# Optimization experiments

Hardware: AMD Instinct MI355X
Metric: run time of the kernel (lower is better)

The kernel has to match this reference:

```python
import jax, jax.numpy as jnp
import numpy as np

N_EMBD = 2048
NUM_GROUPS = 8
EXPERTS_PER_GROUP = 8
ROUTER_TEMPERATURE = 1.0
N_TOKENS = 16384


def setup_inputs() -> dict:
    key = jax.random.key(0)
    kx, kg, ke = jax.random.split(key, 3)
    x = jax.random.normal(kx, (N_TOKENS, N_EMBD), dtype=jnp.float32)
    # nn.Linear(in, out, bias=False) stores weight as [out, in]; kaiming-uniform-ish scale
    bound = 1.0 / np.sqrt(N_EMBD)
    group_gate_w = jax.random.uniform(kg, (NUM_GROUPS, N_EMBD), dtype=jnp.float32,
                                      minval=-bound, maxval=bound)
    expert_gate_w = jax.random.uniform(ke, (NUM_GROUPS * EXPERTS_PER_GROUP, N_EMBD),
                                       dtype=jnp.float32, minval=-bound, maxval=bound)
    return {"x": x, "group_gate_w": group_gate_w, "expert_gate_w": expert_gate_w}


def reference(x, group_gate_w, expert_gate_w):
    N = x.shape[0]
    G = NUM_GROUPS
    E_g = EXPERTS_PER_GROUP
    inv_temp = 1.0 / ROUTER_TEMPERATURE

    # Level 1: group routing
    group_logits = jnp.einsum('nd,gd->ng', x, group_gate_w)            # [N, G]
    group_probs = jax.nn.softmax(group_logits * inv_temp, axis=-1)     # [N, G]
    group_mask = group_probs >= (1.0 / G)                              # [N, G]

    # Level 2: expert routing within each group
    expert_logits = jnp.einsum('nd,ed->ne', x, expert_gate_w)          # [N, G*E_g]
    expert_logits = expert_logits.reshape(N, G, E_g)
    expert_probs = jax.nn.softmax(expert_logits * inv_temp, axis=-1)   # [N, G, E_g]
    expert_mask = expert_probs >= (1.0 / E_g)                          # [N, G, E_g]

    valid_mask_3d = group_mask[:, :, None] & expert_mask               # [N, G, E_g]
    selected_weights_3d = (group_probs[:, :, None] * expert_probs) * valid_mask_3d.astype(x.dtype)

    valid_mask = valid_mask_3d.reshape(N, G * E_g)
    selected_weights = selected_weights_3d.reshape(N, G * E_g)
    weight_sum = jnp.clip(jnp.sum(selected_weights, axis=-1, keepdims=True), 1e-9, None)
    normalized_weights = selected_weights / weight_sum
    return (valid_mask, normalized_weights)
```

## Files before the change

kernel.cpp:

```cpp
#include <hip/hip_runtime.h>


#define NT 16384
#define NE 2048
#define NTH 256
#define NBLK 512
#define NCHUNK 16
#define KSB 10240
#define WCH 40960
#define LDS_BYTES 81920

typedef _Float16 v8h __attribute__((ext_vector_type(8)));
typedef float    v4f __attribute__((ext_vector_type(4)));

__global__ __launch_bounds__(256, 1)
void prep(const float* __restrict__ gw, const float* __restrict__ ew,
          _Float16* __restrict__ wf)
{
    const int t = blockIdx.x * 256 + threadIdx.x;
    const int j    = t & 7;
    const int sl   = (t >> 3) & 63;
    const int rest = t >> 9;
    const int g    = rest % 5;
    const int ks   = rest / 5;
    const int m = sl & 15, q = sl >> 4;
    const int gate = g * 16 + m;
    const int k = ks * 32 + q * 8 + j;
    float v = 0.f;
    if (gate < 64)      v = ew[gate * NE + k];
    else if (gate < 72) v = gw[(gate - 64) * NE + k];
    const _Float16 h = (_Float16)v;
    const int o = (((ks * 5 + g) * 2) * 64 + sl) * 8 + j;
    wf[o]       = h;
    wf[o + 512] = (_Float16)((v - (float)h) * 2048.0f);
}

__global__ __launch_bounds__(NTH, 2)
void router(const float* __restrict__ x, const _Float16* __restrict__ wf,
            float* __restrict__ out)
{
    __shared__ __align__(16) char sm[LDS_BYTES];
    const int tid  = threadIdx.x;
    const int lane = tid & 63;
    const int w    = tid >> 6;
    const int t0   = blockIdx.x * 32;

    const float* xq0 = x + (size_t)(t0 + (lane & 15)) * NE + w * 32 + (lane >> 4) * 8;
    const float* xq1 = xq0 + (size_t)16 * NE;

    auto stage = [&](int c, int buf) {
        const char* src = (const char*)wf + (size_t)c * WCH + w * KSB + lane * 16;
        char* dst = sm + buf * WCH + w * KSB;
        #pragma unroll
        for (int i = 0; i < 10; ++i)
            __builtin_amdgcn_global_load_lds(
                (const __attribute__((address_space(1))) char*)(src + i * 1024),
                (__attribute__((address_space(3))) char*)(dst + i * 1024),
                16, 0, 0);
    };

    auto split8 = [](const float4& a, const float4& b, v8h& h, v8h& l) {
        const float v[8] = {a.x, a.y, a.z, a.w, b.x, b.y, b.z, b.w};
        #pragma unroll
        for (int j = 0; j < 8; ++j) {
            const _Float16 hh = (_Float16)v[j];
            h[j] = hh;
            l[j] = (_Float16)((v[j] - (float)hh) * 2048.0f);
        }
    };

    v4f accH0[5], accC0[5], accH1[5], accC1[5];
    #pragma unroll
    for (int g = 0; g < 5; ++g) {
        accH0[g] = (v4f)(0.f); accC0[g] = (v4f)(0.f);
        accH1[g] = (v4f)(0.f); accC1[g] = (v4f)(0.f);
    }

    auto xload = [&](int c, float4& a0, float4& a1, float4& b0, float4& b1) {
        const float* p0 = xq0 + c * 128;
        const float* p1 = xq1 + c * 128;
        a0 = *(const float4*)(p0); a1 = *(const float4*)(p0 + 4);
        b0 = *(const float4*)(p1); b1 = *(const float4*)(p1 + 4);
    };

    auto step = [&](int c, int P, float4& c00, float4& c01, float4& c10, float4& c11) {
        __syncthreads();
        if (c + 1 < NCHUNK) stage(c + 1, 1 - P);
        v8h Bh0, Bl0, Bh1, Bl1;
        split8(c00, c01, Bh0, Bl0);
        split8(c10, c11, Bh1, Bl1);
        if (c + 2 < NCHUNK) xload(c + 2, c00, c01, c10, c11);
        const char* wb = sm + P * WCH + w * KSB + lane * 16;
        #pragma unroll
        for (int g = 0; g < 5; ++g) {
            const v8h Ah = *(const v8h*)(wb + g * 2048);
            const v8h Al = *(const v8h*)(wb + g * 2048 + 1024);
            accH0[g] = __builtin_amdgcn_mfma_f32_16x16x32_f16(Ah, Bh0, accH0[g], 0, 0, 0);
            accC0[g] = __builtin_amdgcn_mfma_f32_16x16x32_f16(Ah, Bl0, accC0[g], 0, 0, 0);
            accC0[g] = __builtin_amdgcn_mfma_f32_16x16x32_f16(Al, Bh0, accC0[g], 0, 0, 0);
            accH1[g] = __builtin_amdgcn_mfma_f32_16x16x32_f16(Ah, Bh1, accH1[g], 0, 0, 0);
            accC1[g] = __builtin_amdgcn_mfma_f32_16x16x32_f16(Ah, Bl1, accC1[g], 0, 0, 0);
            accC1[g] = __builtin_amdgcn_mfma_f32_16x16x32_f16(Al, Bh1, accC1[g], 0, 0, 0);
        }
    };

    float4 xA00, xA01, xA10, xA11, xB00, xB01, xB10, xB11;

    stage(0, 0);
    xload(0, xA00, xA01, xA10, xA11);
    xload(1, xB00, xB01, xB10, xB11);

    #pragma unroll 1
    for (int cc = 0; cc < NCHUNK; cc += 2) {
        step(cc,     0, xA00, xA01, xA10, xA11);
        step(cc + 1, 1, xB00, xB01, xB10, xB11);
    }
    __syncthreads();

    float part[2][5][4];
    #pragma unroll
    for (int g = 0; g < 5; ++g)
        #pragma unroll
        for (int r = 0; r < 4; ++r) {
            part[0][g][r] = accH0[g][r] + accC0[g][r] * (1.0f / 2048.0f);
            part[1][g][r] = accH1[g][r] + accC1[g][r] * (1.0f / 2048.0f);
        }

    float* red = (float*)sm;
    if (w > 0) {
        #pragma unroll
        for (int t = 0; t < 2; ++t)
            #pragma unroll
            for (int g = 0; g < 5; ++g)
                #pragma unroll
                for (int r = 0; r < 4; ++r)
                    red[((((w - 1) * 2 + t) * 5 + g) * 4 + r) * 64 + lane] = part[t][g][r];
    }
    __syncthreads();
    float* la = (float*)(sm + 30720);
    if (w == 0) {
        #pragma unroll
        for (int t = 0; t < 2; ++t)
            #pragma unroll
            for (int g = 0; g < 5; ++g)
                #pragma unroll
                for (int r = 0; r < 4; ++r) {
                    const float v = part[t][g][r]
                        + red[(((0 * 2 + t) * 5 + g) * 4 + r) * 64 + lane]
                        + red[(((1 * 2 + t) * 5 + g) * 4 + r) * 64 + lane]
                        + red[(((2 * 2 + t) * 5 + g) * 4 + r) * 64 + lane];
                    const int gate  = g * 16 + (lane >> 4) * 4 + r;
                    const int token = t * 16 + (lane & 15);
                    la[token * 84 + gate] = v;
                }
    }
    __syncthreads();

    if (lane < 8) {
        const int token = w * 8 + lane;
        const float* lg = la + token * 84;
        float* M  = (float*)(sm + 41472) + token * 64;
        float* Wn = (float*)(sm + 49664) + token * 64;

        float gpb[8];
        float gmax = lg[64];
        #pragma unroll
        for (int g = 1; g < 8; ++g) gmax = fmaxf(gmax, lg[64 + g]);
        float gsum = 0.f;
        #pragma unroll
        for (int g = 0; g < 8; ++g) { gpb[g] = __expf(lg[64 + g] - gmax); gsum += gpb[g]; }
        const float ginv = 1.f / gsum;

        float sel[64];
        float wsum = 0.f;
        #pragma unroll
        for (int g = 0; g < 8; ++g) {
            const float gp_ = gpb[g] * ginv;
            float emax = lg[g * 8];
            #pragma unroll
            for (int j = 1; j < 8; ++j) emax = fmaxf(emax, lg[g * 8 + j]);
            float ep[8]; float esum = 0.f;
            #pragma unroll
            for (int j = 0; j < 8; ++j) { ep[j] = __expf(lg[g * 8 + j] - emax); esum += ep[j]; }
            const float einv = 1.f / esum;
            const bool gm = gp_ >= 0.125f;
            #pragma unroll
            for (int j = 0; j < 8; ++j) {
                const float pe = ep[j] * einv;
                const bool v = gm && (pe >= 0.125f);
                const float ww = v ? gp_ * pe : 0.f;
                M[g * 8 + j] = v ? 1.f : 0.f;
                sel[g * 8 + j] = ww;
                wsum += ww;
            }
        }
        const float inv = 1.f / fmaxf(wsum, 1e-9f);
        #pragma unroll
        for (int e = 0; e < 64; ++e) Wn[e] = sel[e] * inv;
    }
    __syncthreads();

    const float4* M4 = (const float4*)(sm + 41472);
    const float4* W4 = (const float4*)(sm + 49664);
    float4* o0 = (float4*)(out + (size_t)t0 * 64);
    float4* o1 = (float4*)(out + (size_t)NT * 64 + (size_t)t0 * 64);
    o0[tid]       = M4[tid];
    o0[tid + 256] = M4[tid + 256];
    o1[tid]       = W4[tid];
    o1[tid + 256] = W4[tid + 256];
}

extern "C" void kernel_launch(void* const* d_in, const int* in_sizes, int n_in,
                              void* d_out, int out_size, void* d_ws, size_t ws_size,
                              hipStream_t stream) {
    const float* x  = (const float*)d_in[0];
    const float* gw = (const float*)d_in[1];
    const float* ew = (const float*)d_in[2];
    float* out = (float*)d_out;
    _Float16* wf = (_Float16*)d_ws;
    (void)ws_size; (void)in_sizes; (void)n_in; (void)out_size;

    prep<<<dim3(640), dim3(256), 0, stream>>>(gw, ew, wf);
    router<<<dim3(NBLK), dim3(NTH), 0, stream>>>(x, wf, out);
}
```

Before: 205.5 us.

## Replace per-chunk block barriers with per-wave vmcnt waits in the GEMM loop

Each wave stages and reads only its own slice of the LDS weight buffer. The block-wide __syncthreads in every chunk step is therefore dropped and replaced by explicit s_waitcnt vmcnt counts fenced with sched_barrier. The x prefetch and LDS staging are issued before the wait, and the last two chunks are peeled off so the wait counts stay exact. The aim is to remove barrier stalls and let waves drift apart to overlap loads with MFMA work, at the cost of depending on hand-tuned counter values being correct.

After: 211.0 us. 1.03x slower.

```diff
diff --git a/kernel.cpp b/kernel.cpp
--- a/kernel.cpp
+++ b/kernel.cpp
@@ -83,13 +83,8 @@
         b0 = *(const float4*)(p1); b1 = *(const float4*)(p1 + 4);
     };
 
-    auto step = [&](int c, int P, float4& c00, float4& c01, float4& c10, float4& c11) {
-        __syncthreads();
-        if (c + 1 < NCHUNK) stage(c + 1, 1 - P);
-        v8h Bh0, Bl0, Bh1, Bl1;
-        split8(c00, c01, Bh0, Bl0);
-        split8(c10, c11, Bh1, Bl1);
-        if (c + 2 < NCHUNK) xload(c + 2, c00, c01, c10, c11);
+    auto mfma_block = [&](int P, const v8h& Bh0, const v8h& Bl0,
+                          const v8h& Bh1, const v8h& Bl1) {
         const char* wb = sm + P * WCH + w * KSB + lane * 16;
         #pragma unroll
         for (int g = 0; g < 5; ++g) {
@@ -104,16 +99,47 @@
         }
     };
 
+    auto step = [&](int c, int P, float4& c00, float4& c01, float4& c10, float4& c11) {
+        v8h Bh0, Bl0, Bh1, Bl1;
+        split8(c00, c01, Bh0, Bl0);
+        split8(c10, c11, Bh1, Bl1);
+        xload(c + 2, c00, c01, c10, c11);
+        stage(c + 1, 1 - P);
+        __builtin_amdgcn_sched_barrier(0);
+        asm volatile("s_waitcnt vmcnt(14)" ::: "memory");
+        __builtin_amdgcn_sched_barrier(0);
+        mfma_block(P, Bh0, Bl0, Bh1, Bl1);
+    };
+
     float4 xA00, xA01, xA10, xA11, xB00, xB01, xB10, xB11;
 
-    stage(0, 0);
     xload(0, xA00, xA01, xA10, xA11);
     xload(1, xB00, xB01, xB10, xB11);
+    stage(0, 0);
 
     #pragma unroll 1
-    for (int cc = 0; cc < NCHUNK; cc += 2) {
+    for (int cc = 0; cc < NCHUNK - 2; cc += 2) {
         step(cc,     0, xA00, xA01, xA10, xA11);
         step(cc + 1, 1, xB00, xB01, xB10, xB11);
+    }
+    {
+        v8h Bh0, Bl0, Bh1, Bl1;
+        split8(xA00, xA01, Bh0, Bl0);
+        split8(xA10, xA11, Bh1, Bl1);
+        stage(15, 1);
+        __builtin_amdgcn_sched_barrier(0);
+        asm volatile("s_waitcnt vmcnt(10)" ::: "memory");
+        __builtin_amdgcn_sched_barrier(0);
+        mfma_block(0, Bh0, Bl0, Bh1, Bl1);
+    }
+    {
+        v8h Bh0, Bl0, Bh1, Bl1;
+        split8(xB00, xB01, Bh0, Bl0);
+        split8(xB10, xB11, Bh1, Bl1);
+        __builtin_amdgcn_sched_barrier(0);
+        asm volatile("s_waitcnt vmcnt(0)" ::: "memory");
+        __builtin_amdgcn_sched_barrier(0);
+        mfma_block(1, Bh0, Bl0, Bh1, Bl1);
     }
     __syncthreads();
 
```
